# Optimization experiments

Hardware: AMD Instinct MI355X
Metric: run time of the kernel (lower is better)

## Reference

```python
import jax, jax.numpy as jnp
import numpy as np

B, C, H, W = 4, 512, 64, 64
CK = C // 8  # key/query channels


def setup_inputs() -> dict:
    key = jax.random.key(0)
    ks = jax.random.split(key, 4)
    x = jax.random.normal(ks[0], (B, C, H, W), dtype=jnp.float32)
    # 1x1 conv weights -> plain [out, in] matrices; fan-in scaled like torch default-ish
    Wf = jax.random.normal(ks[1], (CK, C), dtype=jnp.float32) * (1.0 / np.sqrt(C))
    Wg = jax.random.normal(ks[2], (CK, C), dtype=jnp.float32) * (1.0 / np.sqrt(C))
    Wh = jax.random.normal(ks[3], (C, C), dtype=jnp.float32) * (1.0 / np.sqrt(C))
    bf = jnp.zeros((CK,), dtype=jnp.float32)
    bg = jnp.zeros((CK,), dtype=jnp.float32)
    bh = jnp.zeros((C,), dtype=jnp.float32)
    gamma = jnp.zeros((1,), dtype=jnp.float32)
    return {"x": x, "Wf": Wf, "bf": bf, "Wg": Wg, "bg": bg, "Wh": Wh, "bh": bh, "gamma": gamma}


def reference(x, Wf, bf, Wg, bg, Wh, bh, gamma):
    b, c, h, w = x.shape
    n = h * w
    xf = x.reshape(b, c, n)  # [B, C, N]
    # 1x1 convs == per-pixel linear maps
    f = jnp.einsum('kc,bcn->bkn', Wf, xf) + bf[None, :, None]  # [B, CK, N]
    g = jnp.einsum('kc,bcn->bkn', Wg, xf) + bg[None, :, None]  # [B, CK, N]
    hx = jnp.einsum('oc,bcn->bon', Wh, xf) + bh[None, :, None]  # [B, C, N]
    # energy[b,i,j] = sum_k f[b,k,i] * g[b,k,j]  (f_x.permute(0,2,1) @ g_x)
    energy = jnp.einsum('bki,bkj->bij', f, g)  # [B, N, N]
    attention = jax.nn.softmax(energy, axis=-1)
    # out[b,c,i] = sum_j hx[b,c,j] * attention[b,i,j]  (h_x @ attention^T)
    out = jnp.einsum('bcj,bij->bci', hx, attention)  # [B, C, N]
    out = out.reshape(b, c, h, w)
    return gamma[0] * out + x
```

## Files before the change

### kernel.cpp

```cpp
#include <hip/hip_runtime.h>
#include <hip/hip_bf16.h>

#define NB 4
#define CC 512
#define NN 4096
#define CKK 64

typedef _Float16 f16x4 __attribute__((ext_vector_type(4)));
typedef _Float16 f16x8 __attribute__((ext_vector_type(8)));
typedef float    f32x4 __attribute__((ext_vector_type(4)));

__device__ __forceinline__ void g2l16(const _Float16* g, _Float16* l) {
    __builtin_amdgcn_global_load_lds(
        (const __attribute__((address_space(1))) void*)g,
        (__attribute__((address_space(3))) void*)l, 16, 0, 0);
}

__device__ __forceinline__ void stage_tile(const _Float16* __restrict__ g, int ldg,
                                           _Float16* lds, int lane, int wave) {
    #pragma unroll
    for (int r = 0; r < 2; r++) {
        int q = r * 4 + wave;
        int row = q * 16 + (lane >> 2);
        int col = (lane & 3) * 8;
        g2l16(g + (size_t)row * ldg + col, lds + q * 512 + lane * 8);
    }
}

__launch_bounds__(256)
__global__ void convert_w(const float* __restrict__ Wf, const float* __restrict__ bf_,
                          const float* __restrict__ Wg, const float* __restrict__ bg_,
                          const float* __restrict__ Wh, const float* __restrict__ bh_,
                          _Float16* __restrict__ Wall, float* __restrict__ Ball) {
    int o = blockIdx.x;
    int t = threadIdx.x;
    const float* src;
    if (o < 64)       src = Wf + (size_t)o * CC;
    else if (o < 128) src = Wg + (size_t)(o - 64) * CC;
    else              src = Wh + (size_t)(o - 128) * CC;
    Wall[(size_t)o * CC + t]       = (_Float16)src[t];
    Wall[(size_t)o * CC + 256 + t] = (_Float16)src[256 + t];
    if (t == 0)
        Ball[o] = (o < 64) ? bf_[o] : (o < 128 ? bg_[o - 64] : bh_[o - 128]);
}

__launch_bounds__(256)
__global__ void proj_mfma(const float* __restrict__ x, const _Float16* __restrict__ Wall,
                          const float* __restrict__ Ball,
                          _Float16* __restrict__ Ft, _Float16* __restrict__ Gt,
                          _Float16* __restrict__ Hx) {
    const int N = NN, C = CC;
    int n0 = blockIdx.x * 128;
    int o0 = blockIdx.y * 128;
    int b  = blockIdx.z;
    const float* xb = x + (size_t)b * C * N;
    __shared__ _Float16 As[128 * 32];
    __shared__ _Float16 Bs[32 * 128];
    int tid = threadIdx.x, lane = tid & 63, wave = tid >> 6;
    int wm = wave & 1, wn = wave >> 1, lrow = lane & 15, quad = lane >> 4;
    int bk = tid >> 3;
    int bs = tid & 7;
    f32x4 acc[4][4] = {};
    for (int kc = 0; kc < C; kc += 32) {
        __syncthreads();
        stage_tile(Wall + (size_t)o0 * C + kc, C, As, lane, wave);
        const float* xr = xb + (size_t)(kc + bk) * N + n0 + bs * 16;
        float4 v0 = *(const float4*)(xr);
        float4 v1 = *(const float4*)(xr + 4);
        float4 v2 = *(const float4*)(xr + 8);
        float4 v3 = *(const float4*)(xr + 12);
        f16x8 h0 = { (_Float16)v0.x, (_Float16)v0.y, (_Float16)v0.z, (_Float16)v0.w,
                     (_Float16)v1.x, (_Float16)v1.y, (_Float16)v1.z, (_Float16)v1.w };
        f16x8 h1 = { (_Float16)v2.x, (_Float16)v2.y, (_Float16)v2.z, (_Float16)v2.w,
                     (_Float16)v3.x, (_Float16)v3.y, (_Float16)v3.z, (_Float16)v3.w };
        *(f16x8*)(Bs + bk * 128 + bs * 16)     = h0;
        *(f16x8*)(Bs + bk * 128 + bs * 16 + 8) = h1;
        __syncthreads();
        f16x8 af[4], bfr[4];
        #pragma unroll
        for (int mi = 0; mi < 4; mi++)
            af[mi] = *(const f16x8*)(As + (wm * 64 + mi * 16 + lrow) * 32 + quad * 8);
        #pragma unroll
        for (int ni = 0; ni < 4; ni++) {
            int n = wn * 64 + ni * 16 + lrow;
            #pragma unroll
            for (int j = 0; j < 8; j++)
                bfr[ni][j] = Bs[(quad * 8 + j) * 128 + n];
        }
        #pragma unroll
        for (int mi = 0; mi < 4; mi++)
            #pragma unroll
            for (int ni = 0; ni < 4; ni++)
                acc[mi][ni] = __builtin_amdgcn_mfma_f32_16x16x32_f16(af[mi], bfr[ni], acc[mi][ni], 0, 0, 0);
    }
    float bias_r[4][4];
    #pragma unroll
    for (int mi = 0; mi < 4; mi++)
        #pragma unroll
        for (int r = 0; r < 4; r++)
            bias_r[mi][r] = Ball[o0 + wm * 64 + mi * 16 + quad * 4 + r];
    _Float16* Ftb = Ft + (size_t)b * NN * CKK;
    _Float16* Gtb = Gt + (size_t)b * NN * CKK;
    _Float16* Hxb = Hx + (size_t)b * CC * N;
    #pragma unroll
    for (int mi = 0; mi < 4; mi++)
        #pragma unroll
        for (int ni = 0; ni < 4; ni++)
            #pragma unroll
            for (int r = 0; r < 4; r++) {
                int o = o0 + wm * 64 + mi * 16 + quad * 4 + r;
                int n = n0 + wn * 64 + ni * 16 + lrow;
                _Float16 v = (_Float16)(acc[mi][ni][r] + bias_r[mi][r]);
                if (o < 64)       Ftb[(size_t)n * CKK + o] = v;
                else if (o < 128) Gtb[(size_t)n * CKK + (o - 64)] = v;
                else              Hxb[(size_t)(o - 128) * N + n] = v;
            }
}

__device__ __forceinline__ void energy_tile_mfma(const _Float16* Arow, const _Float16* Brow,
                                                 _Float16* As, _Float16* Bs,
                                                 int lane, int wave, int wm, int wn,
                                                 int lrow, int quad, f32x4 acc[4][4]) {
    #pragma unroll
    for (int kc = 0; kc < CKK; kc += 32) {
        __syncthreads();
        stage_tile(Arow + kc, CKK, As, lane, wave);
        stage_tile(Brow + kc, CKK, Bs, lane, wave);
        __syncthreads();
        f16x8 af[4], bf[4];
        #pragma unroll
        for (int mi = 0; mi < 4; mi++)
            af[mi] = *(const f16x8*)(As + (wm * 64 + mi * 16 + lrow) * 32 + quad * 8);
        #pragma unroll
        for (int ni = 0; ni < 4; ni++)
            bf[ni] = *(const f16x8*)(Bs + (wn * 64 + ni * 16 + lrow) * 32 + quad * 8);
        #pragma unroll
        for (int mi = 0; mi < 4; mi++)
            #pragma unroll
            for (int ni = 0; ni < 4; ni++)
                acc[mi][ni] = __builtin_amdgcn_mfma_f32_16x16x32_f16(af[mi], bf[ni], acc[mi][ni], 0, 0, 0);
    }
}

__launch_bounds__(256)
__global__ void energy_stats(const _Float16* __restrict__ Ft, const _Float16* __restrict__ Gt,
                             float* __restrict__ Mpart, float* __restrict__ Lpart,
                             int r0, int Rstr) {
    const int N = NN;
    int b = blockIdx.z;
    const _Float16* Arow = Ft + (size_t)b * N * CKK + (size_t)(r0 + blockIdx.y * 128) * CKK;
    const _Float16* Brow = Gt + (size_t)b * N * CKK + (size_t)(blockIdx.x * 128) * CKK;
    __shared__ _Float16 As[128 * 32];
    __shared__ _Float16 Bs[128 * 32];
    __shared__ float Sred[640];
    int tid = threadIdx.x, lane = tid & 63, wave = tid >> 6;
    int wm = wave & 1, wn = wave >> 1, lrow = lane & 15, quad = lane >> 4;
    f32x4 acc[4][4] = {};
    energy_tile_mfma(Arow, Brow, As, Bs, lane, wave, wm, wn, lrow, quad, acc);
    float mloc[16];
    #pragma unroll
    for (int mi = 0; mi < 4; mi++)
        #pragma unroll
        for (int r = 0; r < 4; r++) {
            float v = acc[mi][0][r];
            #pragma unroll
            for (int ni = 1; ni < 4; ni++) v = fmaxf(v, acc[mi][ni][r]);
            mloc[mi * 4 + r] = v;
        }
    #pragma unroll
    for (int off = 1; off < 16; off <<= 1)
        #pragma unroll
        for (int s = 0; s < 16; s++)
            mloc[s] = fmaxf(mloc[s], __shfl_xor(mloc[s], off));
    {
        float v = mloc[0];
        #pragma unroll
        for (int s = 1; s < 16; s++) v = (lrow == s) ? mloc[s] : v;
        int row = wm * 64 + (lrow >> 2) * 16 + quad * 4 + (lrow & 3);
        Sred[wn * 128 + row] = v;
    }
    __syncthreads();
    if (tid < 128) Sred[512 + tid] = fmaxf(Sred[tid], Sred[128 + tid]);
    __syncthreads();
    float lloc[16];
    #pragma unroll
    for (int mi = 0; mi < 4; mi++)
        #pragma unroll
        for (int r = 0; r < 4; r++) {
            int row = wm * 64 + mi * 16 + quad * 4 + r;
            float m = Sred[512 + row];
            float s = 0.f;
            #pragma unroll
            for (int ni = 0; ni < 4; ni++)
                s += __expf((float)(_Float16)acc[mi][ni][r] - m);
            lloc[mi * 4 + r] = s;
        }
    #pragma unroll
    for (int off = 1; off < 16; off <<= 1)
        #pragma unroll
        for (int s = 0; s < 16; s++)
            lloc[s] += __shfl_xor(lloc[s], off);
    {
        float v = lloc[0];
        #pragma unroll
        for (int s = 1; s < 16; s++) v = (lrow == s) ? lloc[s] : v;
        int row = wm * 64 + (lrow >> 2) * 16 + quad * 4 + (lrow & 3);
        Sred[256 + wn * 128 + row] = v;
    }
    __syncthreads();
    if (tid < 128) {
        size_t sidx = ((size_t)b * 32 + blockIdx.x) * Rstr + blockIdx.y * 128 + tid;
        Mpart[sidx] = Sred[512 + tid];
        Lpart[sidx] = Sred[256 + tid] + Sred[256 + 128 + tid];
    }
}

__launch_bounds__(256)
__global__ void combine_stats(const float* __restrict__ Mpart, const float* __restrict__ Lpart,
                              float* __restrict__ Mrow, float* __restrict__ Linv,
                              int rows, int Rstr) {
    int b = blockIdx.y;
    int i = blockIdx.x * 256 + threadIdx.x;
    if (i >= rows) return;
    const float* mp = Mpart + (size_t)b * 32 * Rstr + i;
    const float* lp = Lpart + (size_t)b * 32 * Rstr + i;
    float m = -1e30f;
    #pragma unroll
    for (int jt = 0; jt < 32; jt++) m = fmaxf(m, mp[(size_t)jt * Rstr]);
    float l = 0.f;
    #pragma unroll
    for (int jt = 0; jt < 32; jt++)
        l += lp[(size_t)jt * Rstr] * __expf(mp[(size_t)jt * Rstr] - m);
    Mrow[(size_t)b * Rstr + i] = m;
    Linv[(size_t)b * Rstr + i] = 1.0f / l;
}

__launch_bounds__(256)
__global__ void energy_norm(const _Float16* __restrict__ Ft, const _Float16* __restrict__ Gt,
                            const float* __restrict__ Mrow, const float* __restrict__ Linv,
                            _Float16* __restrict__ P, int r0, int Rstr) {
    const int N = NN;
    int b = blockIdx.z;
    int i0l = blockIdx.y * 128;
    const _Float16* Arow = Ft + (size_t)b * N * CKK + (size_t)(r0 + i0l) * CKK;
    const _Float16* Brow = Gt + (size_t)b * N * CKK + (size_t)(blockIdx.x * 128) * CKK;
    _Float16* Pb = P + (size_t)b * Rstr * N + (size_t)i0l * N + blockIdx.x * 128;
    __shared__ _Float16 As[128 * 32];
    __shared__ _Float16 Bs[128 * 32];
    __shared__ float Sm[128];
    __shared__ float Sl[128];
    int tid = threadIdx.x, lane = tid & 63, wave = tid >> 6;
    int wm = wave & 1, wn = wave >> 1, lrow = lane & 15, quad = lane >> 4;
    if (tid < 128) {
        Sm[tid] = Mrow[(size_t)b * Rstr + i0l + tid];
        Sl[tid] = Linv[(size_t)b * Rstr + i0l + tid];
    }
    f32x4 acc[4][4] = {};
    energy_tile_mfma(Arow, Brow, As, Bs, lane, wave, wm, wn, lrow, quad, acc);
    #pragma unroll
    for (int mi = 0; mi < 4; mi++)
        #pragma unroll
        for (int r = 0; r < 4; r++) {
            int il = wm * 64 + mi * 16 + quad * 4 + r;
            float m = Sm[il], li = Sl[il];
            #pragma unroll
            for (int ni = 0; ni < 4; ni++) {
                int j = wn * 64 + ni * 16 + lrow;
                float p = __expf((float)(_Float16)acc[mi][ni][r] - m) * li;
                Pb[(size_t)il * N + j] = (_Float16)p;
            }
        }
}

__launch_bounds__(256)
__global__ void out_mfma(const _Float16* __restrict__ Hx, const _Float16* __restrict__ P,
                         const float* __restrict__ x, const float* __restrict__ gamma,
                         float* __restrict__ out, int r0, int Rstr) {
    const int N = NN, C = CC;
    int b = blockIdx.z;
    int i0l = blockIdx.x * 128;
    int c0  = blockIdx.y * 128;
    const _Float16* Arow = Hx + (size_t)b * C * N + (size_t)c0 * N;
    const _Float16* Brow = P  + (size_t)b * Rstr * N + (size_t)i0l * N;
    __shared__ _Float16 As[128 * 32];
    __shared__ _Float16 Bs[128 * 32];
    int tid = threadIdx.x, lane = tid & 63, wave = tid >> 6;
    int wm = wave & 1, wn = wave >> 1, lrow = lane & 15, quad = lane >> 4;
    f32x4 acc[4][4] = {};
    for (int kc = 0; kc < N; kc += 32) {
        __syncthreads();
        stage_tile(Arow + kc, N, As, lane, wave);
        stage_tile(Brow + kc, N, Bs, lane, wave);
        __syncthreads();
        f16x8 af[4], bf[4];
        #pragma unroll
        for (int mi = 0; mi < 4; mi++)
            af[mi] = *(const f16x8*)(As + (wm * 64 + mi * 16 + lrow) * 32 + quad * 8);
        #pragma unroll
        for (int ni = 0; ni < 4; ni++)
            bf[ni] = *(const f16x8*)(Bs + (wn * 64 + ni * 16 + lrow) * 32 + quad * 8);
        #pragma unroll
        for (int mi = 0; mi < 4; mi++)
            #pragma unroll
            for (int ni = 0; ni < 4; ni++)
                acc[mi][ni] = __builtin_amdgcn_mfma_f32_16x16x32_f16(af[mi], bf[ni], acc[mi][ni], 0, 0, 0);
    }
    float gv = gamma[0];
    const float* xb = x + (size_t)b * C * N;
    float* ob = out + (size_t)b * C * N;
    int ig0 = r0 + i0l;
    #pragma unroll
    for (int mi = 0; mi < 4; mi++)
        #pragma unroll
        for (int ni = 0; ni < 4; ni++)
            #pragma unroll
            for (int r = 0; r < 4; r++) {
                int c = c0 + wm * 64 + mi * 16 + quad * 4 + r;
                int i = ig0 + wn * 64 + ni * 16 + lrow;
                ob[(size_t)c * N + i] = gv * acc[mi][ni][r] + xb[(size_t)c * N + i];
            }
}

extern "C" void kernel_launch(void* const* d_in, const int* in_sizes, int n_in,
                              void* d_out, int out_size, void* d_ws, size_t ws_size,
                              hipStream_t stream) {
    const float* x     = (const float*)d_in[0];
    const float* Wf    = (const float*)d_in[1];
    const float* bf    = (const float*)d_in[2];
    const float* Wg    = (const float*)d_in[3];
    const float* bg    = (const float*)d_in[4];
    const float* Wh    = (const float*)d_in[5];
    const float* bh    = (const float*)d_in[6];
    const float* gamma = (const float*)d_in[7];
    float* out = (float*)d_out;

    const int B = NB, C = CC, N = NN;

    char* wsb = (char*)d_ws;
    _Float16* Wall = (_Float16*)wsb;
    float*    Ball = (float*)(wsb + ((size_t)768 << 10));
    _Float16* Ft = (_Float16*)(wsb + ((size_t)1 << 20));
    _Float16* Gt = (_Float16*)(wsb + ((size_t)3 << 20));
    _Float16* Hx = (_Float16*)(wsb + ((size_t)5 << 20));
    float* Mpart = (float*)(wsb + ((size_t)21 << 20));
    float* Lpart = (float*)(wsb + ((size_t)23 << 20));
    float* Mrow  = (float*)(wsb + ((size_t)25 << 20));
    float* Linv  = (float*)(wsb + ((size_t)25 << 20) + ((size_t)512 << 10));
    _Float16* P  = (_Float16*)(wsb + ((size_t)26 << 20));
    size_t base = (size_t)26 << 20;
    size_t avail = (ws_size > base) ? ws_size - base : 0;
    size_t bytesPer128 = (size_t)B * N * 2 * 128;
    int R = (int)(avail / bytesPer128) * 128;
    if (R > N) R = N;
    if (R < 128) R = 128;

    convert_w<<<dim3(640), dim3(256), 0, stream>>>(Wf, bf, Wg, bg, Wh, bh, Wall, Ball);
    proj_mfma<<<dim3(N / 128, 5, B), dim3(256), 0, stream>>>(x, Wall, Ball, Ft, Gt, Hx);

    for (int r0 = 0; r0 < N; r0 += R) {
        int rows = (R < N - r0) ? R : (N - r0);
        energy_stats<<<dim3(N / 128, rows / 128, B), dim3(256), 0, stream>>>(
            Ft, Gt, Mpart, Lpart, r0, R);
        combine_stats<<<dim3((rows + 255) / 256, B), dim3(256), 0, stream>>>(
            Mpart, Lpart, Mrow, Linv, rows, R);
        energy_norm<<<dim3(N / 128, rows / 128, B), dim3(256), 0, stream>>>(
            Ft, Gt, Mrow, Linv, P, r0, R);
        out_mfma<<<dim3(rows / 128, C / 128, B), dim3(256), 0, stream>>>(
            Hx, P, x, gamma, out, r0, R);
    }
}
```

Before: 291.6 us.

## Fuse energy stats and normalization; rescale P per tile in output GEMM

The separate stats and normalization passes over the energy matrix become one pass that writes unnormalized tile-local exp values along with per-tile max and sum. combine_stats now emits per-tile correction factors, and the output GEMM applies them to the P operand as it loads it, which removes the second energy GEMM and exp pass. The projection input x is also pre-transposed into fp16, so the projection GEMM stages both operands with direct global-to-LDS loads instead of scalar strided LDS reads. The cost is an extra transpose kernel, per-element fp16 multiplies in the inner loop of out_mfma, and some precision risk from storing tile-local exponentials in fp16.

New measurement: 271.3 us. 7.0% less time.

```diff
diff --git a/kernel.cpp b/kernel.cpp
--- a/kernel.cpp
+++ b/kernel.cpp
@@ -25,6 +25,30 @@
         int col = (lane & 3) * 8;
         g2l16(g + (size_t)row * ldg + col, lds + q * 512 + lane * 8);
     }
+}
+
+__launch_bounds__(256)
+__global__ void transpose_x(const float* __restrict__ x, _Float16* __restrict__ xT) {
+    const int N = NN, C = CC;
+    int n0 = blockIdx.x * 64, c0 = blockIdx.y * 64, b = blockIdx.z;
+    __shared__ float T[64][65];
+    int t = threadIdx.x;
+    const float* xb = x + (size_t)b * C * N;
+    #pragma unroll
+    for (int r = 0; r < 4; r++) {
+        int c = (t >> 4) + 16 * r;
+        int n4 = (t & 15) * 4;
+        float4 v = *(const float4*)(xb + (size_t)(c0 + c) * N + n0 + n4);
+        T[n4 + 0][c] = v.x; T[n4 + 1][c] = v.y; T[n4 + 2][c] = v.z; T[n4 + 3][c] = v.w;
+    }
+    __syncthreads();
+    int n = t >> 2, cb = (t & 3) * 16;
+    f16x8 h0, h1;
+    #pragma unroll
+    for (int i = 0; i < 8; i++) { h0[i] = (_Float16)T[n][cb + i]; h1[i] = (_Float16)T[n][cb + 8 + i]; }
+    _Float16* dst = xT + (size_t)b * N * C + (size_t)(n0 + n) * C + c0 + cb;
+    *(f16x8*)dst = h0;
+    *(f16x8*)(dst + 8) = h1;
 }
 
 __launch_bounds__(256)
@@ -45,7 +69,7 @@
 }
 
 __launch_bounds__(256)
-__global__ void proj_mfma(const float* __restrict__ x, const _Float16* __restrict__ Wall,
+__global__ void proj_mfma(const _Float16* __restrict__ xT, const _Float16* __restrict__ Wall,
                           const float* __restrict__ Ball,
                           _Float16* __restrict__ Ft, _Float16* __restrict__ Gt,
                           _Float16* __restrict__ Hx) {
@@ -53,45 +77,30 @@
     int n0 = blockIdx.x * 128;
     int o0 = blockIdx.y * 128;
     int b  = blockIdx.z;
-    const float* xb = x + (size_t)b * C * N;
+    const _Float16* Arow = Wall + (size_t)o0 * C;
+    const _Float16* Brow = xT + (size_t)b * N * C + (size_t)n0 * C;
     __shared__ _Float16 As[128 * 32];
-    __shared__ _Float16 Bs[32 * 128];
+    __shared__ _Float16 Bs[128 * 32];
     int tid = threadIdx.x, lane = tid & 63, wave = tid >> 6;
     int wm = wave & 1, wn = wave >> 1, lrow = lane & 15, quad = lane >> 4;
-    int bk = tid >> 3;
-    int bs = tid & 7;
     f32x4 acc[4][4] = {};
     for (int kc = 0; kc < C; kc += 32) {
         __syncthreads();
-        stage_tile(Wall + (size_t)o0 * C + kc, C, As, lane, wave);
-        const float* xr = xb + (size_t)(kc + bk) * N + n0 + bs * 16;
-        float4 v0 = *(const float4*)(xr);
-        float4 v1 = *(const float4*)(xr + 4);
-        float4 v2 = *(const float4*)(xr + 8);
-        float4 v3 = *(const float4*)(xr + 12);
-        f16x8 h0 = { (_Float16)v0.x, (_Float16)v0.y, (_Float16)v0.z, (_Float16)v0.w,
-                     (_Float16)v1.x, (_Float16)v1.y, (_Float16)v1.z, (_Float16)v1.w };
-        f16x8 h1 = { (_Float16)v2.x, (_Float16)v2.y, (_Float16)v2.z, (_Float16)v2.w,
-                     (_Float16)v3.x, (_Float16)v3.y, (_Float16)v3.z, (_Float16)v3.w };
-        *(f16x8*)(Bs + bk * 128 + bs * 16)     = h0;
-        *(f16x8*)(Bs + bk * 128 + bs * 16 + 8) = h1;
+        stage_tile(Arow + kc, C, As, lane, wave);
+        stage_tile(Brow + kc, C, Bs, lane, wave);
         __syncthreads();
-        f16x8 af[4], bfr[4];
+        f16x8 af[4], bf[4];
         #pragma unroll
         for (int mi = 0; mi < 4; mi++)
             af[mi] = *(const f16x8*)(As + (wm * 64 + mi * 16 + lrow) * 32 + quad * 8);
         #pragma unroll
-        for (int ni = 0; ni < 4; ni++) {
-            int n = wn * 64 + ni * 16 + lrow;
-            #pragma unroll
-            for (int j = 0; j < 8; j++)
-                bfr[ni][j] = Bs[(quad * 8 + j) * 128 + n];
-        }
+        for (int ni = 0; ni < 4; ni++)
+            bf[ni] = *(const f16x8*)(Bs + (wn * 64 + ni * 16 + lrow) * 32 + quad * 8);
         #pragma unroll
         for (int mi = 0; mi < 4; mi++)
             #pragma unroll
             for (int ni = 0; ni < 4; ni++)
-                acc[mi][ni] = __builtin_amdgcn_mfma_f32_16x16x32_f16(af[mi], bfr[ni], acc[mi][ni], 0, 0, 0);
+                acc[mi][ni] = __builtin_amdgcn_mfma_f32_16x16x32_f16(af[mi], bf[ni], acc[mi][ni], 0, 0, 0);
     }
     float bias_r[4][4];
     #pragma unroll
@@ -117,10 +126,21 @@
             }
 }
 
-__device__ __forceinline__ void energy_tile_mfma(const _Float16* Arow, const _Float16* Brow,
-                                                 _Float16* As, _Float16* Bs,
-                                                 int lane, int wave, int wm, int wn,
-                                                 int lrow, int quad, f32x4 acc[4][4]) {
+__launch_bounds__(256)
+__global__ void energy_fused(const _Float16* __restrict__ Ft, const _Float16* __restrict__ Gt,
+                             _Float16* __restrict__ P, float* __restrict__ Mpart,
+                             float* __restrict__ Lpart, int r0, int Rstr) {
+    const int N = NN;
+    int b = blockIdx.z;
+    const _Float16* Arow = Ft + (size_t)b * N * CKK + (size_t)(r0 + blockIdx.y * 128) * CKK;
+    const _Float16* Brow = Gt + (size_t)b * N * CKK + (size_t)(blockIdx.x * 128) * CKK;
+    _Float16* Pb = P + (size_t)b * Rstr * N + (size_t)blockIdx.y * 128 * N + blockIdx.x * 128;
+    __shared__ _Float16 As[128 * 32];
+    __shared__ _Float16 Bs[128 * 32];
+    __shared__ float Sred[640];
+    int tid = threadIdx.x, lane = tid & 63, wave = tid >> 6;
+    int wm = wave & 1, wn = wave >> 1, lrow = lane & 15, quad = lane >> 4;
+    f32x4 acc[4][4] = {};
     #pragma unroll
     for (int kc = 0; kc < CKK; kc += 32) {
         __syncthreads();
@@ -140,23 +160,6 @@
             for (int ni = 0; ni < 4; ni++)
                 acc[mi][ni] = __builtin_amdgcn_mfma_f32_16x16x32_f16(af[mi], bf[ni], acc[mi][ni], 0, 0, 0);
     }
-}
-
-__launch_bounds__(256)
-__global__ void energy_stats(const _Float16* __restrict__ Ft, const _Float16* __restrict__ Gt,
-                             float* __restrict__ Mpart, float* __restrict__ Lpart,
-                             int r0, int Rstr) {
-    const int N = NN;
-    int b = blockIdx.z;
-    const _Float16* Arow = Ft + (size_t)b * N * CKK + (size_t)(r0 + blockIdx.y * 128) * CKK;
-    const _Float16* Brow = Gt + (size_t)b * N * CKK + (size_t)(blockIdx.x * 128) * CKK;
-    __shared__ _Float16 As[128 * 32];
-    __shared__ _Float16 Bs[128 * 32];
-    __shared__ float Sred[640];
-    int tid = threadIdx.x, lane = tid & 63, wave = tid >> 6;
-    int wm = wave & 1, wn = wave >> 1, lrow = lane & 15, quad = lane >> 4;
-    f32x4 acc[4][4] = {};
-    energy_tile_mfma(Arow, Brow, As, Bs, lane, wave, wm, wn, lrow, quad, acc);
     float mloc[16];
     #pragma unroll
     for (int mi = 0; mi < 4; mi++)
@@ -191,8 +194,13 @@
             float m = Sred[512 + row];
             float s = 0.f;
             #pragma unroll
-            for (int ni = 0; ni < 4; ni++)
-                s += __expf((float)(_Float16)acc[mi][ni][r] - m);
+            for (int ni = 0; ni < 4; ni++) {
+                int j = wn * 64 + ni * 16 + lrow;
+                float s16 = (float)(_Float16)acc[mi][ni][r];
+                _Float16 p16 = (_Float16)__expf(s16 - m);
+                Pb[(size_t)row * N + j] = p16;
+                s += (float)p16;
+            }
             lloc[mi * 4 + r] = s;
         }
     #pragma unroll
@@ -217,8 +225,7 @@
 
 __launch_bounds__(256)
 __global__ void combine_stats(const float* __restrict__ Mpart, const float* __restrict__ Lpart,
-                              float* __restrict__ Mrow, float* __restrict__ Linv,
-                              int rows, int Rstr) {
+                              _Float16* __restrict__ cfac, int rows, int Rstr) {
     int b = blockIdx.y;
     int i = blockIdx.x * 256 + threadIdx.x;
     if (i >= rows) return;
@@ -231,49 +238,16 @@
     #pragma unroll
     for (int jt = 0; jt < 32; jt++)
         l += lp[(size_t)jt * Rstr] * __expf(mp[(size_t)jt * Rstr] - m);
-    Mrow[(size_t)b * Rstr + i] = m;
-    Linv[(size_t)b * Rstr + i] = 1.0f / l;
-}
-
-__launch_bounds__(256)
-__global__ void energy_norm(const _Float16* __restrict__ Ft, const _Float16* __restrict__ Gt,
-                            const float* __restrict__ Mrow, const float* __restrict__ Linv,
-                            _Float16* __restrict__ P, int r0, int Rstr) {
-    const int N = NN;
-    int b = blockIdx.z;
-    int i0l = blockIdx.y * 128;
-    const _Float16* Arow = Ft + (size_t)b * N * CKK + (size_t)(r0 + i0l) * CKK;
-    const _Float16* Brow = Gt + (size_t)b * N * CKK + (size_t)(blockIdx.x * 128) * CKK;
-    _Float16* Pb = P + (size_t)b * Rstr * N + (size_t)i0l * N + blockIdx.x * 128;
-    __shared__ _Float16 As[128 * 32];
-    __shared__ _Float16 Bs[128 * 32];
-    __shared__ float Sm[128];
-    __shared__ float Sl[128];
-    int tid = threadIdx.x, lane = tid & 63, wave = tid >> 6;
-    int wm = wave & 1, wn = wave >> 1, lrow = lane & 15, quad = lane >> 4;
-    if (tid < 128) {
-        Sm[tid] = Mrow[(size_t)b * Rstr + i0l + tid];
-        Sl[tid] = Linv[(size_t)b * Rstr + i0l + tid];
-    }
-    f32x4 acc[4][4] = {};
-    energy_tile_mfma(Arow, Brow, As, Bs, lane, wave, wm, wn, lrow, quad, acc);
-    #pragma unroll
-    for (int mi = 0; mi < 4; mi++)
-        #pragma unroll
-        for (int r = 0; r < 4; r++) {
-            int il = wm * 64 + mi * 16 + quad * 4 + r;
-            float m = Sm[il], li = Sl[il];
-            #pragma unroll
-            for (int ni = 0; ni < 4; ni++) {
-                int j = wn * 64 + ni * 16 + lrow;
-                float p = __expf((float)(_Float16)acc[mi][ni][r] - m) * li;
-                Pb[(size_t)il * N + j] = (_Float16)p;
-            }
-        }
+    float linv = 1.0f / l;
+    _Float16* cf = cfac + (size_t)b * 32 * Rstr + i;
+    #pragma unroll
+    for (int jt = 0; jt < 32; jt++)
+        cf[(size_t)jt * Rstr] = (_Float16)(__expf(mp[(size_t)jt * Rstr] - m) * linv);
 }
 
 __launch_bounds__(256)
 __global__ void out_mfma(const _Float16* __restrict__ Hx, const _Float16* __restrict__ P,
+                         const _Float16* __restrict__ cfac,
                          const float* __restrict__ x, const float* __restrict__ gamma,
                          float* __restrict__ out, int r0, int Rstr) {
     const int N = NN, C = CC;
@@ -284,26 +258,45 @@
     const _Float16* Brow = P  + (size_t)b * Rstr * N + (size_t)i0l * N;
     __shared__ _Float16 As[128 * 32];
     __shared__ _Float16 Bs[128 * 32];
+    __shared__ _Float16 Cf[32 * 128];
     int tid = threadIdx.x, lane = tid & 63, wave = tid >> 6;
     int wm = wave & 1, wn = wave >> 1, lrow = lane & 15, quad = lane >> 4;
+    #pragma unroll
+    for (int r = 0; r < 16; r++) {
+        int idx = tid + r * 256;
+        int jt = idx >> 7, ii = idx & 127;
+        Cf[idx] = cfac[((size_t)b * 32 + jt) * Rstr + i0l + ii];
+    }
+    __syncthreads();
     f32x4 acc[4][4] = {};
-    for (int kc = 0; kc < N; kc += 32) {
-        __syncthreads();
-        stage_tile(Arow + kc, N, As, lane, wave);
-        stage_tile(Brow + kc, N, Bs, lane, wave);
-        __syncthreads();
-        f16x8 af[4], bf[4];
-        #pragma unroll
-        for (int mi = 0; mi < 4; mi++)
-            af[mi] = *(const f16x8*)(As + (wm * 64 + mi * 16 + lrow) * 32 + quad * 8);
-        #pragma unroll
-        for (int ni = 0; ni < 4; ni++)
-            bf[ni] = *(const f16x8*)(Bs + (wn * 64 + ni * 16 + lrow) * 32 + quad * 8);
-        #pragma unroll
-        for (int mi = 0; mi < 4; mi++)
-            #pragma unroll
-            for (int ni = 0; ni < 4; ni++)
-                acc[mi][ni] = __builtin_amdgcn_mfma_f32_16x16x32_f16(af[mi], bf[ni], acc[mi][ni], 0, 0, 0);
+    for (int jt = 0; jt < 32; jt++) {
+        _Float16 cfv[4];
+        #pragma unroll
+        for (int ni = 0; ni < 4; ni++)
+            cfv[ni] = Cf[jt * 128 + wn * 64 + ni * 16 + lrow];
+        #pragma unroll
+        for (int kk = 0; kk < 4; kk++) {
+            int kc = jt * 128 + kk * 32;
+            __syncthreads();
+            stage_tile(Arow + kc, N, As, lane, wave);
+            stage_tile(Brow + kc, N, Bs, lane, wave);
+            __syncthreads();
+            f16x8 af[4], bf[4];
+            #pragma unroll
+            for (int mi = 0; mi < 4; mi++)
+                af[mi] = *(const f16x8*)(As + (wm * 64 + mi * 16 + lrow) * 32 + quad * 8);
+            #pragma unroll
+            for (int ni = 0; ni < 4; ni++) {
+                bf[ni] = *(const f16x8*)(Bs + (wn * 64 + ni * 16 + lrow) * 32 + quad * 8);
+                #pragma unroll
+                for (int j = 0; j < 8; j++) bf[ni][j] *= cfv[ni];
+            }
+            #pragma unroll
+            for (int mi = 0; mi < 4; mi++)
+                #pragma unroll
+                for (int ni = 0; ni < 4; ni++)
+                    acc[mi][ni] = __builtin_amdgcn_mfma_f32_16x16x32_f16(af[mi], bf[ni], acc[mi][ni], 0, 0, 0);
+        }
     }
     float gv = gamma[0];
     const float* xb = x + (size_t)b * C * N;
@@ -344,9 +337,9 @@
     _Float16* Hx = (_Float16*)(wsb + ((size_t)5 << 20));
     float* Mpart = (float*)(wsb + ((size_t)21 << 20));
     float* Lpart = (float*)(wsb + ((size_t)23 << 20));
-    float* Mrow  = (float*)(wsb + ((size_t)25 << 20));
-    float* Linv  = (float*)(wsb + ((size_t)25 << 20) + ((size_t)512 << 10));
+    _Float16* cfac = (_Float16*)(wsb + ((size_t)25 << 20));
     _Float16* P  = (_Float16*)(wsb + ((size_t)26 << 20));
+    _Float16* xT = P;
     size_t base = (size_t)26 << 20;
     size_t avail = (ws_size > base) ? ws_size - base : 0;
     size_t bytesPer128 = (size_t)B * N * 2 * 128;
@@ -354,18 +347,17 @@
     if (R > N) R = N;
     if (R < 128) R = 128;
 
+    transpose_x<<<dim3(N / 64, C / 64, B), dim3(256), 0, stream>>>(x, xT);
     convert_w<<<dim3(640), dim3(256), 0, stream>>>(Wf, bf, Wg, bg, Wh, bh, Wall, Ball);
-    proj_mfma<<<dim3(N / 128, 5, B), dim3(256), 0, stream>>>(x, Wall, Ball, Ft, Gt, Hx);
+    proj_mfma<<<dim3(N / 128, 5, B), dim3(256), 0, stream>>>(xT, Wall, Ball, Ft, Gt, Hx);
 
     for (int r0 = 0; r0 < N; r0 += R) {
         int rows = (R < N - r0) ? R : (N - r0);
-        energy_stats<<<dim3(N / 128, rows / 128, B), dim3(256), 0, stream>>>(
-            Ft, Gt, Mpart, Lpart, r0, R);
+        energy_fused<<<dim3(N / 128, rows / 128, B), dim3(256), 0, stream>>>(
+            Ft, Gt, P, Mpart, Lpart, r0, R);
         combine_stats<<<dim3((rows + 255) / 256, B), dim3(256), 0, stream>>>(
-            Mpart, Lpart, Mrow, Linv, rows, R);
-        energy_norm<<<dim3(N / 128, rows / 128, B), dim3(256), 0, stream>>>(
-            Ft, Gt, Mrow, Linv, P, r0, R);
+            Mpart, Lpart, cfac, rows, R);
         out_mfma<<<dim3(rows / 128, C / 128, B), dim3(256), 0, stream>>>(
-            Hx, P, x, gamma, out, r0, R);
-    }
-}
+            Hx, P, cfac, x, gamma, out, r0, R);
+    }
+}
```
